# Optimization experiments

Hardware: AMD Instinct MI355X
Metric: run time of the kernel (lower is better)

## Reference

```python
import jax, jax.numpy as jnp
import numpy as np

V, D, H, L, T_BLOCK = 32000, 1024, 16, 4, 1024
HD = D // H
FF = 4 * D
EPS = 1e-5


def layer_norm(x, w, b):
    mu = jnp.mean(x, axis=-1, keepdims=True)
    var = jnp.mean(jnp.square(x - mu), axis=-1, keepdims=True)
    return (x - mu) * jax.lax.rsqrt(var + EPS) * w + b


def setup_inputs() -> dict:
    key = jax.random.key(0)
    ks = iter(jax.random.split(key, 32))
    s = 0.02
    inp = {
        "idx": jax.random.randint(next(ks), (4, 1024), 0, V, dtype=jnp.int32),
        "tok_emb": jax.random.normal(next(ks), (V, D), jnp.float32) * s,
        "pos_emb": jax.random.normal(next(ks), (T_BLOCK, D), jnp.float32) * s,
        "ln1_w": jnp.ones((L, D), jnp.float32),
        "ln1_b": jnp.zeros((L, D), jnp.float32),
        "wq": jax.random.normal(next(ks), (L, D, D), jnp.float32) * s,
        "wk": jax.random.normal(next(ks), (L, D, D), jnp.float32) * s,
        "wv": jax.random.normal(next(ks), (L, D, D), jnp.float32) * s,
        "wproj": jax.random.normal(next(ks), (L, D, D), jnp.float32) * s,
        "bproj": jnp.zeros((L, D), jnp.float32),
        "ln2_w": jnp.ones((L, D), jnp.float32),
        "ln2_b": jnp.zeros((L, D), jnp.float32),
        "w1": jax.random.normal(next(ks), (L, D, FF), jnp.float32) * s,
        "b1": jnp.zeros((L, FF), jnp.float32),
        "w2": jax.random.normal(next(ks), (L, FF, D), jnp.float32) * s,
        "b2": jnp.zeros((L, D), jnp.float32),
        "lnf_w": jnp.ones((D,), jnp.float32),
        "lnf_b": jnp.zeros((D,), jnp.float32),
        "wout": jax.random.normal(next(ks), (D, V), jnp.float32) * s,
        "bout": jnp.zeros((V,), jnp.float32),
    }
    return inp


def reference(idx, tok_emb, pos_emb, ln1_w, ln1_b, wq, wk, wv, wproj, bproj,
              ln2_w, ln2_b, w1, b1, w2, b2, lnf_w, lnf_b, wout, bout):
    B, T = idx.shape
    x = tok_emb[idx] + pos_emb[:T]  # (B,T,D)
    causal = jnp.tril(jnp.ones((T, T), bool))
    scale = 1.0 / jnp.sqrt(jnp.asarray(HD, x.dtype))
    for l in range(L):
        h = layer_norm(x, ln1_w[l], ln1_b[l])
        q = (h @ wq[l]).reshape(B, T, H, HD)
        k = (h @ wk[l]).reshape(B, T, H, HD)
        v = (h @ wv[l]).reshape(B, T, H, HD)
        scores = jnp.einsum('bqhd,bkhd->bhqk', q, k) * scale
        scores = jnp.where(causal, scores, -jnp.inf)
        weights = jax.nn.softmax(scores, axis=-1)
        attn = jnp.einsum('bhqk,bkhd->bqhd', weights, v).reshape(B, T, D)
        x = x + attn @ wproj[l] + bproj[l]
        h2 = layer_norm(x, ln2_w[l], ln2_b[l])
        x = x + jax.nn.relu(h2 @ w1[l] + b1[l]) @ w2[l] + b2[l]
    x = layer_norm(x, lnf_w, lnf_b)
    logits = x @ wout + bout  # (B,T,V)
    return logits
```

## Files before the change

### kernel.cpp

```cpp
#include <hip/hip_runtime.h>
#include <hip/hip_bf16.h>

#define V_  32000
#define D_  1024
#define H_  16
#define L_  4
#define T_  1024
#define B_  4
#define HD_ 64
#define FF_ 4096
#define M_  4096
#define QP_ 3072

typedef unsigned short u16;
typedef float  f32x4   __attribute__((ext_vector_type(4)));
typedef float  f32x16  __attribute__((ext_vector_type(16)));
typedef __bf16 bf16x8  __attribute__((ext_vector_type(8)));
typedef u16    us8     __attribute__((ext_vector_type(8)));

typedef __attribute__((address_space(1))) void gvoid;
typedef __attribute__((address_space(3))) void lvoid;

__device__ __forceinline__ void glds16(const void* g, void* l) {
  __builtin_amdgcn_global_load_lds((gvoid*)g, (lvoid*)l, 16, 0, 0);
}
__device__ __forceinline__ u16 f2bf(float f) {
  __hip_bfloat16 h = __float2bfloat16(f);
  return reinterpret_cast<u16&>(h);
}

__global__ __launch_bounds__(256) void embed_kernel(
    const int* __restrict__ idx, const float* __restrict__ tok,
    const float* __restrict__ pos, float* __restrict__ x)
{
  int bt = blockIdx.x;
  int t  = bt & (T_ - 1);
  int id = idx[bt];
  float4 a = ((const float4*)(tok + (size_t)id * D_))[threadIdx.x];
  float4 p = ((const float4*)(pos + (size_t)t  * D_))[threadIdx.x];
  a.x += p.x; a.y += p.y; a.z += p.z; a.w += p.w;
  ((float4*)(x + (size_t)bt * D_))[threadIdx.x] = a;
}

__global__ __launch_bounds__(256) void ln_kernel(
    const float* __restrict__ x, const float* __restrict__ w,
    const float* __restrict__ b, u16* __restrict__ out)
{
  int row = blockIdx.x;
  float4 v = ((const float4*)(x + (size_t)row * D_))[threadIdx.x];
  float s  = v.x + v.y + v.z + v.w;
  float s2 = v.x * v.x + v.y * v.y + v.z * v.z + v.w * v.w;
#pragma unroll
  for (int m = 1; m < 64; m <<= 1) { s += __shfl_xor(s, m); s2 += __shfl_xor(s2, m); }
  __shared__ float ssum[4], ssum2[4];
  int wv = threadIdx.x >> 6;
  if ((threadIdx.x & 63) == 0) { ssum[wv] = s; ssum2[wv] = s2; }
  __syncthreads();
  s  = ssum[0]  + ssum[1]  + ssum[2]  + ssum[3];
  s2 = ssum2[0] + ssum2[1] + ssum2[2] + ssum2[3];
  float mu  = s * (1.f / D_);
  float var = s2 * (1.f / D_) - mu * mu;
  float rs  = rsqrtf(var + 1e-5f);
  float4 wv4 = ((const float4*)w)[threadIdx.x];
  float4 bv4 = ((const float4*)b)[threadIdx.x];
  u16* o = out + (size_t)row * D_ + threadIdx.x * 4;
  o[0] = f2bf((v.x - mu) * rs * wv4.x + bv4.x);
  o[1] = f2bf((v.y - mu) * rs * wv4.y + bv4.y);
  o[2] = f2bf((v.z - mu) * rs * wv4.z + bv4.z);
  o[3] = f2bf((v.w - mu) * rs * wv4.w + bv4.w);
}

__global__ __launch_bounds__(256) void transpose_convert(
    const float* __restrict__ in, u16* __restrict__ out, int R, int C,
    size_t inStride, size_t outStride)
{
  __shared__ float tile[32][33];
  in  += (size_t)blockIdx.z * inStride;
  out += (size_t)blockIdx.z * outStride;
  int c  = blockIdx.x * 32 + threadIdx.x;
  int r0 = blockIdx.y * 32;
#pragma unroll
  for (int j = 0; j < 4; j++)
    tile[threadIdx.y + 8 * j][threadIdx.x] =
        in[(size_t)(r0 + threadIdx.y + 8 * j) * C + c];
  __syncthreads();
  int rr = r0 + threadIdx.x;
  int cb = blockIdx.x * 32;
#pragma unroll
  for (int j = 0; j < 4; j++)
    out[(size_t)(cb + threadIdx.y + 8 * j) * R + rr] =
        f2bf(tile[threadIdx.x][threadIdx.y + 8 * j]);
}

__global__ __launch_bounds__(256) void vtrans_kernel(
    const u16* __restrict__ qkv, u16* __restrict__ vtb)
{
  __shared__ u16 tile[64][72];
  int tt = blockIdx.x, bh = blockIdx.y;
  int b = bh >> 4, h = bh & 15;
  const u16* src = qkv + ((size_t)(b * T_ + tt * 64)) * QP_ + 2 * D_ + h * HD_;
#pragma unroll
  for (int it = 0; it < 2; it++) {
    int u = it * 256 + threadIdx.x;
    int r = u >> 3, c = (u & 7) << 3;
    *(us8*)&tile[r][c] = *(const us8*)&src[(size_t)r * QP_ + c];
  }
  __syncthreads();
#pragma unroll
  for (int it = 0; it < 2; it++) {
    int u = it * 256 + threadIdx.x;
    int d = u >> 3, t8 = (u & 7) << 3;
    us8 v;
#pragma unroll
    for (int j = 0; j < 8; j++) v[j] = tile[t8 + j][d];
    *(us8*)&vtb[((size_t)bh * HD_ + d) * T_ + tt * 64 + t8] = v;
  }
}

template<int EPI>
__global__ __launch_bounds__(256) void gemm_bt(
    const u16* __restrict__ A, const u16* __restrict__ Bt,
    const float* __restrict__ bias, const float* __restrict__ resid,
    void* __restrict__ Cout, int M, int N, int K)
{
  __shared__ u16 As[128 * 32];
  __shared__ u16 Bs[128 * 32];
  const int tid = threadIdx.x;
  const int m0 = blockIdx.x * 128;
  const int n0 = blockIdx.y * 128;
  const int w = tid >> 6, lane = tid & 63, lg = lane >> 4, lr = lane & 15;
  const int wr = w >> 1, wc = w & 1;
  f32x4 acc[4][4] = {};
  const int srow = tid >> 2;
  const int scol = (tid & 3) << 3;
  const u16* ap = A  + (size_t)(m0 + srow) * K + scol;
  const u16* bp = Bt + (size_t)(n0 + srow) * K + scol;
  u16* alds  = &As[tid * 8];
  u16* alds2 = &As[2048 + tid * 8];
  u16* blds  = &Bs[tid * 8];
  u16* blds2 = &Bs[2048 + tid * 8];
  for (int k0 = 0; k0 < K; k0 += 32) {
    __syncthreads();
    glds16(ap + k0,                  alds);
    glds16(ap + (size_t)64 * K + k0, alds2);
    glds16(bp + k0,                  blds);
    glds16(bp + (size_t)64 * K + k0, blds2);
    __syncthreads();
    bf16x8 af[4], bfr[4];
#pragma unroll
    for (int i = 0; i < 4; i++)
      af[i] = *(const bf16x8*)&As[(wr * 64 + i * 16 + lr) * 32 + lg * 8];
#pragma unroll
    for (int j = 0; j < 4; j++)
      bfr[j] = *(const bf16x8*)&Bs[(wc * 64 + j * 16 + lr) * 32 + lg * 8];
#pragma unroll
    for (int i = 0; i < 4; i++)
#pragma unroll
      for (int j = 0; j < 4; j++)
        acc[i][j] = __builtin_amdgcn_mfma_f32_16x16x32_bf16(af[i], bfr[j], acc[i][j], 0, 0, 0);
  }
#pragma unroll
  for (int i = 0; i < 4; i++) {
#pragma unroll
    for (int j = 0; j < 4; j++) {
      int col = n0 + wc * 64 + j * 16 + lr;
      float bv = bias ? bias[col] : 0.f;
#pragma unroll
      for (int r = 0; r < 4; r++) {
        int row = m0 + wr * 64 + i * 16 + lg * 4 + r;
        float val = acc[i][j][r] + bv;
        size_t o = (size_t)row * N + col;
        if (EPI == 0)      ((u16*)Cout)[o]   = f2bf(val);
        else if (EPI == 1) ((u16*)Cout)[o]   = f2bf(val > 0.f ? val : 0.f);
        else if (EPI == 2) ((float*)Cout)[o] = resid[o] + val;
        else               ((float*)Cout)[o] = val;
      }
    }
  }
}

#define BAR() __builtin_amdgcn_s_barrier()
#define VMC(n) asm volatile("s_waitcnt vmcnt(" #n ")" ::: "memory")
#define LGKMC(n) do { asm volatile("s_waitcnt lgkmcnt(" #n ")" ::: "memory"); \
                      __builtin_amdgcn_sched_barrier(0); } while (0)

#define CLUSTER(AF, BV, MS) do { \
  __builtin_amdgcn_s_setprio(1); \
  _Pragma("unroll") for (int mq_ = 0; mq_ < 2; ++mq_) \
  _Pragma("unroll") for (int nq_ = 0; nq_ < 2; ++nq_) \
  _Pragma("unroll") for (int kq_ = 0; kq_ < 2; ++kq_) \
    acc[(MS)+mq_][nq_] = __builtin_amdgcn_mfma_f32_32x32x16_bf16( \
        AF[mq_][kq_], BV[nq_][kq_], acc[(MS)+mq_][nq_], 0, 0, 0); \
  __builtin_amdgcn_s_setprio(0); \
} while (0)

template<int EPI>
__global__ __launch_bounds__(512, 2) void gemm256(
    const u16* __restrict__ A, const u16* __restrict__ Bt,
    const float* __restrict__ bias, void* __restrict__ Cout, int N, int K)
{
  extern __shared__ char smem[];
  const int tid = threadIdx.x;
  const int nwg = gridDim.x;
  const int orig = blockIdx.x;
  const int qq = nwg >> 3, rr = nwg & 7, xcd = orig & 7, lid = orig >> 3;
  const int swz = (xcd < rr ? xcd * (qq + 1) : rr * (qq + 1) + (xcd - rr) * qq) + lid;
  const int m0 = (swz & 15) << 8;
  const int n0 = (swz >> 4) << 8;
  const int NT = K >> 6;

  const int wid = tid >> 6, lane = tid & 63;
  const int wr = wid >> 2, wc = wid & 3;
  const int l31 = lane & 31, lh = lane >> 5;
  const int gsw = (lane & 7) ^ ((lane >> 3) & 3);
  const int srow = tid >> 3, sslot = tid & 7;
  const int sg = (srow & 7) ^ ((srow >> 3) & 3);
  const int scol = ((sslot ^ sg) << 3);
  const u16* Ag = A  + (size_t)(m0 + srow) * K + scol;
  const u16* Bg = Bt + (size_t)(n0 + srow) * K + scol;
  char* ldst = smem + tid * 16;

  auto stA = [&](int bb, int kt, int h) {
    const u16* g = Ag + (size_t)(h << 7) * K + (kt << 6);
    char* l = ldst + bb * 65536 + h * 16384;
    glds16(g, l);
    glds16(g + ((size_t)K << 6), l + 8192);
  };
  auto stB = [&](int bb, int kt, int h) {
    const u16* g = Bg + (size_t)(h << 7) * K + (kt << 6);
    char* l = ldst + bb * 65536 + 32768 + h * 16384;
    glds16(g, l);
    glds16(g + ((size_t)K << 6), l + 8192);
  };
  auto ldA = [&](int bb, int mf, int ks) {
    return *(const bf16x8*)(smem + bb * 65536 +
        ((wr * 128 + mf * 32 + l31) << 7) + (((ks * 2 + lh) ^ gsw) << 4));
  };
  auto ldB = [&](int bb, int nf, int ks) {
    return *(const bf16x8*)(smem + bb * 65536 + 32768 +
        ((wc * 64 + nf * 32 + l31) << 7) + (((ks * 2 + lh) ^ gsw) << 4));
  };

  f32x16 acc[4][2] = {};
  bf16x8 afA[2][2], afB[2][2], bfvA[2][2], bfvB[2][2];

  stA(0, 0, 0); stA(0, 0, 1); stB(0, 0, 0); stB(0, 0, 1);
  VMC(0); BAR();

  for (int t = 0; t < NT; ++t) {
    const int bb = t & 1;
    if (t + 1 < NT) {
      stA(bb ^ 1, t + 1, 0); stA(bb ^ 1, t + 1, 1);
      stB(bb ^ 1, t + 1, 0); stB(bb ^ 1, t + 1, 1);
    }
#pragma unroll
    for (int i = 0; i < 2; i++) {
      afA[i][0]  = ldA(bb, i, 0);     afA[i][1]  = ldA(bb, i, 1);
      bfvA[i][0] = ldB(bb, i, 0);     bfvA[i][1] = ldB(bb, i, 1);
    }
#pragma unroll
    for (int i = 0; i < 2; i++) { afB[i][0] = ldA(bb, 2 + i, 0); afB[i][1] = ldA(bb, 2 + i, 1); }
    LGKMC(4);
    CLUSTER(afA, bfvA, 0);
#pragma unroll
    for (int i = 0; i < 2; i++) { bfvB[i][0] = ldB(bb, i, 2); bfvB[i][1] = ldB(bb, i, 3); }
#pragma unroll
    for (int i = 0; i < 2; i++) { afA[i][0] = ldA(bb, i, 2); afA[i][1] = ldA(bb, i, 3); }
    LGKMC(8);
    CLUSTER(afB, bfvA, 2);
#pragma unroll
    for (int i = 0; i < 2; i++) { afB[i][0] = ldA(bb, 2 + i, 2); afB[i][1] = ldA(bb, 2 + i, 3); }
    LGKMC(4);
    CLUSTER(afA, bfvB, 0);
    LGKMC(0);
    CLUSTER(afB, bfvB, 2);
    VMC(0); BAR();
  }

#pragma unroll
  for (int nf = 0; nf < 2; ++nf) {
    const int col = n0 + wc * 64 + nf * 32 + l31;
    const float bv = bias ? bias[col] : 0.f;
#pragma unroll
    for (int mf = 0; mf < 4; ++mf) {
#pragma unroll
      for (int v = 0; v < 16; ++v) {
        const int row = m0 + wr * 128 + mf * 32 + (v & 3) + 8 * (v >> 2) + 4 * lh;
        float val = acc[mf][nf][v] + bv;
        size_t o = (size_t)row * N + col;
        if (EPI == 0)      ((u16*)Cout)[o]   = f2bf(val);
        else if (EPI == 1) ((u16*)Cout)[o]   = f2bf(val > 0.f ? val : 0.f);
        else               ((float*)Cout)[o] = val;
      }
    }
  }
}

__global__ __launch_bounds__(512) void attn_kernel(
    const u16* __restrict__ qkv, const u16* __restrict__ vtb,
    u16* __restrict__ o)
{
  __shared__ u16 Ks[2][64][64];
  __shared__ u16 Vs[2][64][64];
  __shared__ u16 Ps[8][16][72];
  const int qt = blockIdx.x;
  const int bh = blockIdx.y;
  const int b = bh >> 4, h = bh & 15;
  const int tid = threadIdx.x;
  const int w = tid >> 6, lane = tid & 63, lg = lane >> 4, lr = lane & 15;
  const int q0 = qt * 128;
  const size_t qbase = ((size_t)b * T_) * QP_ + h * HD_;
  const size_t obase = ((size_t)b * T_) * D_ + h * HD_;
  const u16* qb = qkv + qbase;
  const u16* kb = qkv + qbase + D_;
  const u16* vtbh = vtb + (size_t)bh * HD_ * T_;
  bf16x8 qf[2];
  const int qrow = q0 + w * 16 + lr;
#pragma unroll
  for (int ks = 0; ks < 2; ks++)
    qf[ks] = *(const bf16x8*)&qb[(size_t)qrow * QP_ + ks * 32 + lg * 8];
  f32x4 oacc[4] = {};
  float mrun[4] = {-1e30f, -1e30f, -1e30f, -1e30f};
  float lrun[4] = {0.f, 0.f, 0.f, 0.f};
  const int srow = tid >> 3, sslot = tid & 7;
  const int sg = (srow & 7) ^ ((srow >> 3) & 3);
  const int scol = (sslot ^ sg) << 3;
  u16* kdst = &Ks[0][0][0] + tid * 8;
  u16* vdst = &Vs[0][0][0] + tid * 8;
  auto stage = [&](int kt, int bb) {
    glds16(kb + (size_t)(kt * 64 + srow) * QP_ + scol, kdst + bb * 4096);
    glds16(vtbh + (size_t)srow * T_ + kt * 64 + scol, vdst + bb * 4096);
  };
  auto ldK = [&](int bb, int j, int ks) {
    int r = j * 16 + lr;
    int g = (r & 7) ^ ((r >> 3) & 3);
    return *(const bf16x8*)&Ks[bb][r][((ks * 4 + lg) ^ g) << 3];
  };
  auto ldV = [&](int bb, int jd, int ks) {
    int r = jd * 16 + lr;
    int g = (r & 7) ^ ((r >> 3) & 3);
    return *(const bf16x8*)&Vs[bb][r][((ks * 4 + lg) ^ g) << 3];
  };

  const int ktmax = 2 * qt + 1;
  stage(0, 0);
  VMC(0); BAR();
  for (int kt = 0; kt <= ktmax; kt++) {
    const int bb = kt & 1;
    if (kt < ktmax) stage(kt + 1, bb ^ 1);
    f32x4 s[4] = {};
#pragma unroll
    for (int ks = 0; ks < 2; ks++)
#pragma unroll
      for (int j = 0; j < 4; j++)
        s[j] = __builtin_amdgcn_mfma_f32_16x16x32_bf16(qf[ks], ldK(bb, j, ks), s[j], 0, 0, 0);
#pragma unroll
    for (int j = 0; j < 4; j++) {
      int key = kt * 64 + j * 16 + lr;
#pragma unroll
      for (int r = 0; r < 4; r++) {
        int qr = q0 + w * 16 + lg * 4 + r;
        s[j][r] = (key <= qr) ? s[j][r] * 0.125f : -1e30f;
      }
    }
    float al[4];
#pragma unroll
    for (int r = 0; r < 4; r++) {
      float t0 = fmaxf(fmaxf(s[0][r], s[1][r]), fmaxf(s[2][r], s[3][r]));
#pragma unroll
      for (int m = 1; m < 16; m <<= 1) t0 = fmaxf(t0, __shfl_xor(t0, m));
      float mnew = fmaxf(mrun[r], t0);
      al[r] = __expf(mrun[r] - mnew);
      mrun[r] = mnew;
    }
#pragma unroll
    for (int j = 0; j < 4; j++)
#pragma unroll
      for (int r = 0; r < 4; r++)
        s[j][r] = __expf(s[j][r] - mrun[r]);
#pragma unroll
    for (int r = 0; r < 4; r++) {
      float rs = s[0][r] + s[1][r] + s[2][r] + s[3][r];
#pragma unroll
      for (int m = 1; m < 16; m <<= 1) rs += __shfl_xor(rs, m);
      lrun[r] = lrun[r] * al[r] + rs;
#pragma unroll
      for (int jd = 0; jd < 4; jd++) oacc[jd][r] *= al[r];
    }
#pragma unroll
    for (int j = 0; j < 4; j++)
#pragma unroll
      for (int r = 0; r < 4; r++)
        Ps[w][lg * 4 + r][j * 16 + lr] = f2bf(s[j][r]);
    asm volatile("s_waitcnt lgkmcnt(0)" ::: "memory");
    __builtin_amdgcn_sched_barrier(0);
#pragma unroll
    for (int ks = 0; ks < 2; ks++) {
      bf16x8 pf = *(const bf16x8*)&Ps[w][lr][ks * 32 + lg * 8];
#pragma unroll
      for (int jd = 0; jd < 4; jd++)
        oacc[jd] = __builtin_amdgcn_mfma_f32_16x16x32_bf16(pf, ldV(bb, jd, ks), oacc[jd], 0, 0, 0);
    }
    VMC(0); BAR();
  }
#pragma unroll
  for (int jd = 0; jd < 4; jd++)
#pragma unroll
    for (int r = 0; r < 4; r++) {
      int row = q0 + w * 16 + lg * 4 + r;
      o[obase + (size_t)row * D_ + jd * 16 + lr] = f2bf(oacc[jd][r] / lrun[r]);
    }
}

extern "C" void kernel_launch(void* const* d_in, const int* in_sizes, int n_in,
                              void* d_out, int out_size, void* d_ws, size_t ws_size,
                              hipStream_t stream)
{
  const int*   idx   = (const int*)  d_in[0];
  const float* tok   = (const float*)d_in[1];
  const float* pos   = (const float*)d_in[2];
  const float* ln1w  = (const float*)d_in[3];
  const float* ln1b  = (const float*)d_in[4];
  const float* wq    = (const float*)d_in[5];
  const float* wk    = (const float*)d_in[6];
  const float* wvw   = (const float*)d_in[7];
  const float* wproj = (const float*)d_in[8];
  const float* bproj = (const float*)d_in[9];
  const float* ln2w  = (const float*)d_in[10];
  const float* ln2b  = (const float*)d_in[11];
  const float* w1    = (const float*)d_in[12];
  const float* b1    = (const float*)d_in[13];
  const float* w2    = (const float*)d_in[14];
  const float* b2    = (const float*)d_in[15];
  const float* lnfw  = (const float*)d_in[16];
  const float* lnfb  = (const float*)d_in[17];
  const float* wout  = (const float*)d_in[18];
  const float* bout  = (const float*)d_in[19];

  hipFuncSetAttribute(reinterpret_cast<const void*>(&gemm256<0>),
                      hipFuncAttributeMaxDynamicSharedMemorySize, 131072);
  hipFuncSetAttribute(reinterpret_cast<const void*>(&gemm256<1>),
                      hipFuncAttributeMaxDynamicSharedMemorySize, 131072);
  hipFuncSetAttribute(reinterpret_cast<const void*>(&gemm256<3>),
                      hipFuncAttributeMaxDynamicSharedMemorySize, 131072);

  char* ws = (char*)d_ws;
  size_t off = 0;
  auto alloc = [&](size_t bytes) {
    void* p = ws + off;
    off += (bytes + 255) & ~(size_t)255;
    return p;
  };
  u16* wqkvT  = (u16*)alloc((size_t)L_ * 3 * D_ * D_ * 2);
  u16* wprojT = (u16*)alloc((size_t)L_ * D_ * D_ * 2);
  u16* w1T    = (u16*)alloc((size_t)L_ * D_ * FF_ * 2);
  u16* w2T    = (u16*)alloc((size_t)L_ * D_ * FF_ * 2);
  u16* woutT  = (u16*)alloc((size_t)D_ * V_ * 2);
  float* x    = (float*)alloc((size_t)M_ * D_ * 4);
  u16* hbuf   = (u16*)alloc((size_t)M_ * D_ * 2);
  u16* qkvbuf = (u16*)alloc((size_t)M_ * QP_ * 2);
  u16* vtb    = (u16*)alloc((size_t)B_ * H_ * HD_ * T_ * 2);
  u16* abuf   = (u16*)alloc((size_t)M_ * D_ * 2);
  u16* f1buf  = (u16*)alloc((size_t)M_ * FF_ * 2);

  dim3 tb(32, 8);
  const size_t DD = (size_t)D_ * D_, DF = (size_t)D_ * FF_;
  transpose_convert<<<dim3(D_ / 32, D_ / 32, L_), tb, 0, stream>>>(wq,    wqkvT,          D_,  D_, DD, 3 * DD);
  transpose_convert<<<dim3(D_ / 32, D_ / 32, L_), tb, 0, stream>>>(wk,    wqkvT + DD,     D_,  D_, DD, 3 * DD);
  transpose_convert<<<dim3(D_ / 32, D_ / 32, L_), tb, 0, stream>>>(wvw,   wqkvT + 2 * DD, D_,  D_, DD, 3 * DD);
  transpose_convert<<<dim3(D_ / 32, D_ / 32, L_), tb, 0, stream>>>(wproj, wprojT,         D_,  D_, DD, DD);
  transpose_convert<<<dim3(FF_ / 32, D_ / 32, L_), tb, 0, stream>>>(w1,   w1T,            D_,  FF_, DF, DF);
  transpose_convert<<<dim3(D_ / 32, FF_ / 32, L_), tb, 0, stream>>>(w2,   w2T,            FF_, D_, DF, DF);
  transpose_convert<<<dim3(V_ / 32, D_ / 32, 1),  tb, 0, stream>>>(wout,  woutT,          D_,  V_, 0, 0);

  embed_kernel<<<M_, 256, 0, stream>>>(idx, tok, pos, x);

  dim3 gD(M_ / 128, D_ / 128);
  for (int l = 0; l < L_; l++) {
    size_t wo = (size_t)l * DD;
    size_t fo = (size_t)l * DF;
    ln_kernel<<<M_, 256, 0, stream>>>(x, ln1w + l * D_, ln1b + l * D_, hbuf);
    gemm256<0><<<dim3(16 * (QP_ / 256)), 512, 131072, stream>>>(
        hbuf, wqkvT + (size_t)l * 3 * DD, nullptr, qkvbuf, QP_, D_);
    vtrans_kernel<<<dim3(T_ / 64, B_ * H_), 256, 0, stream>>>(qkvbuf, vtb);
    attn_kernel<<<dim3(T_ / 128, B_ * H_), 512, 0, stream>>>(qkvbuf, vtb, abuf);
    gemm_bt<2><<<gD, 256, 0, stream>>>(abuf, wprojT + wo, bproj + l * D_, x, x, M_, D_, D_);
    ln_kernel<<<M_, 256, 0, stream>>>(x, ln2w + l * D_, ln2b + l * D_, hbuf);
    gemm256<1><<<dim3(16 * (FF_ / 256)), 512, 131072, stream>>>(
        hbuf, w1T + fo, b1 + l * FF_, f1buf, FF_, D_);
    gemm_bt<2><<<gD, 256, 0, stream>>>(f1buf, w2T + fo, b2 + l * D_, x, x, M_, D_, FF_);
  }
  ln_kernel<<<M_, 256, 0, stream>>>(x, lnfw, lnfb, hbuf);
  gemm256<3><<<dim3(16 * (V_ / 256)), 512, 131072, stream>>>(
      hbuf, woutT, bout, d_out, V_, D_);
}
```

Measured before the change: 1.634 ms.

## Load GEMM A operand directly from global into registers, stage only B in LDS

The 256x256 GEMM kernel stops staging the A tile through shared memory. Each wave now loads its A fragments straight from global memory into registers, prefetching the next K-step between MFMA phases, while only B is double-buffered in LDS. This halves LDS footprint (64KB instead of 128KB) and LDS read traffic. It also switches from 32x32x16 to 16x16x32 MFMA and makes the tile order row-major over N. In exchange, A reads become uncoalesced per-lane global loads that are duplicated across the four waves sharing a row block, and register pressure grows with 32 f32x4 accumulators plus A and B fragments.

```diff
diff --git a/kernel.cpp b/kernel.cpp
--- a/kernel.cpp
+++ b/kernel.cpp
@@ -28,6 +28,11 @@
   __hip_bfloat16 h = __float2bfloat16(f);
   return reinterpret_cast<u16&>(h);
 }
+
+#define BAR() __builtin_amdgcn_s_barrier()
+#define VMC(n) asm volatile("s_waitcnt vmcnt(" #n ")" ::: "memory")
+#define LGKMC(n) do { asm volatile("s_waitcnt lgkmcnt(" #n ")" ::: "memory"); \
+                      __builtin_amdgcn_sched_barrier(0); } while (0)
 
 __global__ __launch_bounds__(256) void embed_kernel(
     const int* __restrict__ idx, const float* __restrict__ tok,
@@ -179,23 +184,8 @@
   }
 }
 
-#define BAR() __builtin_amdgcn_s_barrier()
-#define VMC(n) asm volatile("s_waitcnt vmcnt(" #n ")" ::: "memory")
-#define LGKMC(n) do { asm volatile("s_waitcnt lgkmcnt(" #n ")" ::: "memory"); \
-                      __builtin_amdgcn_sched_barrier(0); } while (0)
-
-#define CLUSTER(AF, BV, MS) do { \
-  __builtin_amdgcn_s_setprio(1); \
-  _Pragma("unroll") for (int mq_ = 0; mq_ < 2; ++mq_) \
-  _Pragma("unroll") for (int nq_ = 0; nq_ < 2; ++nq_) \
-  _Pragma("unroll") for (int kq_ = 0; kq_ < 2; ++kq_) \
-    acc[(MS)+mq_][nq_] = __builtin_amdgcn_mfma_f32_32x32x16_bf16( \
-        AF[mq_][kq_], BV[nq_][kq_], acc[(MS)+mq_][nq_], 0, 0, 0); \
-  __builtin_amdgcn_s_setprio(0); \
-} while (0)
-
 template<int EPI>
-__global__ __launch_bounds__(512, 2) void gemm256(
+__global__ __launch_bounds__(512, 2) void gemm256g(
     const u16* __restrict__ A, const u16* __restrict__ Bt,
     const float* __restrict__ bias, void* __restrict__ Cout, int N, int K)
 {
@@ -205,88 +195,104 @@
   const int orig = blockIdx.x;
   const int qq = nwg >> 3, rr = nwg & 7, xcd = orig & 7, lid = orig >> 3;
   const int swz = (xcd < rr ? xcd * (qq + 1) : rr * (qq + 1) + (xcd - rr) * qq) + lid;
-  const int m0 = (swz & 15) << 8;
-  const int n0 = (swz >> 4) << 8;
+  const unsigned ntiles = (unsigned)N >> 8;
+  const int m0 = (int)((unsigned)swz / ntiles) << 8;
+  const int n0 = (int)((unsigned)swz % ntiles) << 8;
   const int NT = K >> 6;
 
   const int wid = tid >> 6, lane = tid & 63;
   const int wr = wid >> 2, wc = wid & 3;
-  const int l31 = lane & 31, lh = lane >> 5;
-  const int gsw = (lane & 7) ^ ((lane >> 3) & 3);
+  const int l15 = lane & 15, lq = lane >> 4;
+
+  const u16* Arow = A + (size_t)(m0 + wr * 128 + l15) * K + lq * 8;
+
   const int srow = tid >> 3, sslot = tid & 7;
   const int sg = (srow & 7) ^ ((srow >> 3) & 3);
   const int scol = ((sslot ^ sg) << 3);
-  const u16* Ag = A  + (size_t)(m0 + srow) * K + scol;
   const u16* Bg = Bt + (size_t)(n0 + srow) * K + scol;
   char* ldst = smem + tid * 16;
-
-  auto stA = [&](int bb, int kt, int h) {
-    const u16* g = Ag + (size_t)(h << 7) * K + (kt << 6);
-    char* l = ldst + bb * 65536 + h * 16384;
-    glds16(g, l);
-    glds16(g + ((size_t)K << 6), l + 8192);
+  auto stB = [&](int bb, int kt) {
+#pragma unroll
+    for (int j = 0; j < 4; j++)
+      glds16(Bg + (size_t)(j * 64) * K + (kt << 6), ldst + bb * 32768 + j * 8192);
   };
-  auto stB = [&](int bb, int kt, int h) {
-    const u16* g = Bg + (size_t)(h << 7) * K + (kt << 6);
-    char* l = ldst + bb * 65536 + 32768 + h * 16384;
-    glds16(g, l);
-    glds16(g + ((size_t)K << 6), l + 8192);
+  const int brow = wc * 64 + l15;
+  auto ldB = [&](int bb, int nf, int ks) {
+    int r = brow + nf * 16;
+    int g = (r & 7) ^ ((r >> 3) & 3);
+    return *(const bf16x8*)(smem + bb * 32768 + (r << 7) + ((((ks << 2) + lq) ^ g) << 4));
   };
-  auto ldA = [&](int bb, int mf, int ks) {
-    return *(const bf16x8*)(smem + bb * 65536 +
-        ((wr * 128 + mf * 32 + l31) << 7) + (((ks * 2 + lh) ^ gsw) << 4));
-  };
-  auto ldB = [&](int bb, int nf, int ks) {
-    return *(const bf16x8*)(smem + bb * 65536 + 32768 +
-        ((wc * 64 + nf * 32 + l31) << 7) + (((ks * 2 + lh) ^ gsw) << 4));
-  };
-
-  f32x16 acc[4][2] = {};
-  bf16x8 afA[2][2], afB[2][2], bfvA[2][2], bfvB[2][2];
-
-  stA(0, 0, 0); stA(0, 0, 1); stB(0, 0, 0); stB(0, 0, 1);
-  VMC(0); BAR();
+
+  f32x4 acc[8][4] = {};
+  bf16x8 a0[4][2], a1[4][2], bf[4][2];
+
+  stB(0, 0);
+#pragma unroll
+  for (int mf = 0; mf < 4; mf++)
+#pragma unroll
+    for (int ks = 0; ks < 2; ks++) {
+      a0[mf][ks] = *(const bf16x8*)(Arow + (size_t)(mf * 16) * K + ks * 32);
+      a1[mf][ks] = *(const bf16x8*)(Arow + (size_t)((mf + 4) * 16) * K + ks * 32);
+    }
+  VMC(16); BAR();
 
   for (int t = 0; t < NT; ++t) {
     const int bb = t & 1;
-    if (t + 1 < NT) {
-      stA(bb ^ 1, t + 1, 0); stA(bb ^ 1, t + 1, 1);
-      stB(bb ^ 1, t + 1, 0); stB(bb ^ 1, t + 1, 1);
-    }
-#pragma unroll
-    for (int i = 0; i < 2; i++) {
-      afA[i][0]  = ldA(bb, i, 0);     afA[i][1]  = ldA(bb, i, 1);
-      bfvA[i][0] = ldB(bb, i, 0);     bfvA[i][1] = ldB(bb, i, 1);
-    }
-#pragma unroll
-    for (int i = 0; i < 2; i++) { afB[i][0] = ldA(bb, 2 + i, 0); afB[i][1] = ldA(bb, 2 + i, 1); }
-    LGKMC(4);
-    CLUSTER(afA, bfvA, 0);
-#pragma unroll
-    for (int i = 0; i < 2; i++) { bfvB[i][0] = ldB(bb, i, 2); bfvB[i][1] = ldB(bb, i, 3); }
-#pragma unroll
-    for (int i = 0; i < 2; i++) { afA[i][0] = ldA(bb, i, 2); afA[i][1] = ldA(bb, i, 3); }
-    LGKMC(8);
-    CLUSTER(afB, bfvA, 2);
-#pragma unroll
-    for (int i = 0; i < 2; i++) { afB[i][0] = ldA(bb, 2 + i, 2); afB[i][1] = ldA(bb, 2 + i, 3); }
-    LGKMC(4);
-    CLUSTER(afA, bfvB, 0);
+    const bool sn = (t + 1 < NT);
+    if (sn) stB(bb ^ 1, t + 1);
+#pragma unroll
+    for (int nf = 0; nf < 4; nf++)
+#pragma unroll
+      for (int ks = 0; ks < 2; ks++)
+        bf[nf][ks] = ldB(bb, nf, ks);
     LGKMC(0);
-    CLUSTER(afB, bfvB, 2);
-    VMC(0); BAR();
-  }
-
-#pragma unroll
-  for (int nf = 0; nf < 2; ++nf) {
-    const int col = n0 + wc * 64 + nf * 32 + l31;
+    __builtin_amdgcn_s_setprio(1);
+#pragma unroll
+    for (int mf = 0; mf < 4; mf++)
+#pragma unroll
+      for (int nf = 0; nf < 4; nf++)
+#pragma unroll
+        for (int ks = 0; ks < 2; ks++)
+          acc[mf][nf] = __builtin_amdgcn_mfma_f32_16x16x32_bf16(
+              a0[mf][ks], bf[nf][ks], acc[mf][nf], 0, 0, 0);
+    __builtin_amdgcn_s_setprio(0);
+    if (sn) {
+#pragma unroll
+      for (int mf = 0; mf < 4; mf++)
+#pragma unroll
+        for (int ks = 0; ks < 2; ks++)
+          a0[mf][ks] = *(const bf16x8*)(Arow + (size_t)(mf * 16) * K + ((t + 1) << 6) + ks * 32);
+    }
+    __builtin_amdgcn_s_setprio(1);
+#pragma unroll
+    for (int mf = 0; mf < 4; mf++)
+#pragma unroll
+      for (int nf = 0; nf < 4; nf++)
+#pragma unroll
+        for (int ks = 0; ks < 2; ks++)
+          acc[4 + mf][nf] = __builtin_amdgcn_mfma_f32_16x16x32_bf16(
+              a1[mf][ks], bf[nf][ks], acc[4 + mf][nf], 0, 0, 0);
+    __builtin_amdgcn_s_setprio(0);
+    if (sn) {
+#pragma unroll
+      for (int mf = 0; mf < 4; mf++)
+#pragma unroll
+        for (int ks = 0; ks < 2; ks++)
+          a1[mf][ks] = *(const bf16x8*)(Arow + (size_t)((mf + 4) * 16) * K + ((t + 1) << 6) + ks * 32);
+      VMC(16); BAR();
+    }
+  }
+
+#pragma unroll
+  for (int j = 0; j < 4; j++) {
+    const int col = n0 + wc * 64 + j * 16 + l15;
     const float bv = bias ? bias[col] : 0.f;
 #pragma unroll
-    for (int mf = 0; mf < 4; ++mf) {
-#pragma unroll
-      for (int v = 0; v < 16; ++v) {
-        const int row = m0 + wr * 128 + mf * 32 + (v & 3) + 8 * (v >> 2) + 4 * lh;
-        float val = acc[mf][nf][v] + bv;
+    for (int i = 0; i < 8; i++) {
+#pragma unroll
+      for (int r = 0; r < 4; r++) {
+        const int row = m0 + wr * 128 + i * 16 + lq * 4 + r;
+        float val = acc[i][j][r] + bv;
         size_t o = (size_t)row * N + col;
         if (EPI == 0)      ((u16*)Cout)[o]   = f2bf(val);
         else if (EPI == 1) ((u16*)Cout)[o]   = f2bf(val > 0.f ? val : 0.f);
@@ -437,12 +443,12 @@
   const float* wout  = (const float*)d_in[18];
   const float* bout  = (const float*)d_in[19];
 
-  hipFuncSetAttribute(reinterpret_cast<const void*>(&gemm256<0>),
-                      hipFuncAttributeMaxDynamicSharedMemorySize, 131072);
-  hipFuncSetAttribute(reinterpret_cast<const void*>(&gemm256<1>),
-                      hipFuncAttributeMaxDynamicSharedMemorySize, 131072);
-  hipFuncSetAttribute(reinterpret_cast<const void*>(&gemm256<3>),
-                      hipFuncAttributeMaxDynamicSharedMemorySize, 131072);
+  hipFuncSetAttribute(reinterpret_cast<const void*>(&gemm256g<0>),
+                      hipFuncAttributeMaxDynamicSharedMemorySize, 65536);
+  hipFuncSetAttribute(reinterpret_cast<const void*>(&gemm256g<1>),
+                      hipFuncAttributeMaxDynamicSharedMemorySize, 65536);
+  hipFuncSetAttribute(reinterpret_cast<const void*>(&gemm256g<3>),
+                      hipFuncAttributeMaxDynamicSharedMemorySize, 65536);
 
   char* ws = (char*)d_ws;
   size_t off = 0;
@@ -480,17 +486,17 @@
     size_t wo = (size_t)l * DD;
     size_t fo = (size_t)l * DF;
     ln_kernel<<<M_, 256, 0, stream>>>(x, ln1w + l * D_, ln1b + l * D_, hbuf);
-    gemm256<0><<<dim3(16 * (QP_ / 256)), 512, 131072, stream>>>(
+    gemm256g<0><<<dim3(16 * (QP_ / 256)), 512, 65536, stream>>>(
         hbuf, wqkvT + (size_t)l * 3 * DD, nullptr, qkvbuf, QP_, D_);
     vtrans_kernel<<<dim3(T_ / 64, B_ * H_), 256, 0, stream>>>(qkvbuf, vtb);
     attn_kernel<<<dim3(T_ / 128, B_ * H_), 512, 0, stream>>>(qkvbuf, vtb, abuf);
     gemm_bt<2><<<gD, 256, 0, stream>>>(abuf, wprojT + wo, bproj + l * D_, x, x, M_, D_, D_);
     ln_kernel<<<M_, 256, 0, stream>>>(x, ln2w + l * D_, ln2b + l * D_, hbuf);
-    gemm256<1><<<dim3(16 * (FF_ / 256)), 512, 131072, stream>>>(
+    gemm256g<1><<<dim3(16 * (FF_ / 256)), 512, 65536, stream>>>(
         hbuf, w1T + fo, b1 + l * FF_, f1buf, FF_, D_);
     gemm_bt<2><<<gD, 256, 0, stream>>>(f1buf, w2T + fo, b2 + l * D_, x, x, M_, D_, FF_);
   }
   ln_kernel<<<M_, 256, 0, stream>>>(x, lnfw, lnfb, hbuf);
-  gemm256<3><<<dim3(16 * (V_ / 256)), 512, 131072, stream>>>(
+  gemm256g<3><<<dim3(16 * (V_ / 256)), 512, 65536, stream>>>(
       hbuf, woutT, bout, d_out, V_, D_);
 }
```

Result: slower. 2.343 ms (+43.4%).

## Use 4-stage K=32 LDS pipeline in gemm256 instead of double-buffered K=64

Applied to the files above, without the earlier changes.

Rewrites the main GEMM's K loop to use BK=32 tiles with four LDS buffers of 32KB each, prefetching three tiles ahead via global_load_lds and waiting with graded vmcnt. Previously, double buffering with BK=64 waited for the next tile every iteration. The aim is to hide global memory latency better. In exchange there are twice as many barriers per K step, and the interleaved LDS-read/MFMA clusters are replaced by a single load-then-compute phase, which may expose LDS latency.

```diff
diff --git a/kernel.cpp b/kernel.cpp
--- a/kernel.cpp
+++ b/kernel.cpp
@@ -28,6 +28,11 @@
   __hip_bfloat16 h = __float2bfloat16(f);
   return reinterpret_cast<u16&>(h);
 }
+
+#define BAR() __builtin_amdgcn_s_barrier()
+#define VMC(n) asm volatile("s_waitcnt vmcnt(" #n ")" ::: "memory")
+#define LGKMC(n) do { asm volatile("s_waitcnt lgkmcnt(" #n ")" ::: "memory"); \
+                      __builtin_amdgcn_sched_barrier(0); } while (0)
 
 __global__ __launch_bounds__(256) void embed_kernel(
     const int* __restrict__ idx, const float* __restrict__ tok,
@@ -179,21 +184,6 @@
   }
 }
 
-#define BAR() __builtin_amdgcn_s_barrier()
-#define VMC(n) asm volatile("s_waitcnt vmcnt(" #n ")" ::: "memory")
-#define LGKMC(n) do { asm volatile("s_waitcnt lgkmcnt(" #n ")" ::: "memory"); \
-                      __builtin_amdgcn_sched_barrier(0); } while (0)
-
-#define CLUSTER(AF, BV, MS) do { \
-  __builtin_amdgcn_s_setprio(1); \
-  _Pragma("unroll") for (int mq_ = 0; mq_ < 2; ++mq_) \
-  _Pragma("unroll") for (int nq_ = 0; nq_ < 2; ++nq_) \
-  _Pragma("unroll") for (int kq_ = 0; kq_ < 2; ++kq_) \
-    acc[(MS)+mq_][nq_] = __builtin_amdgcn_mfma_f32_32x32x16_bf16( \
-        AF[mq_][kq_], BV[nq_][kq_], acc[(MS)+mq_][nq_], 0, 0, 0); \
-  __builtin_amdgcn_s_setprio(0); \
-} while (0)
-
 template<int EPI>
 __global__ __launch_bounds__(512, 2) void gemm256(
     const u16* __restrict__ A, const u16* __restrict__ Bt,
@@ -207,74 +197,73 @@
   const int swz = (xcd < rr ? xcd * (qq + 1) : rr * (qq + 1) + (xcd - rr) * qq) + lid;
   const int m0 = (swz & 15) << 8;
   const int n0 = (swz >> 4) << 8;
-  const int NT = K >> 6;
+  const int NT = K >> 5;
 
   const int wid = tid >> 6, lane = tid & 63;
   const int wr = wid >> 2, wc = wid & 3;
   const int l31 = lane & 31, lh = lane >> 5;
-  const int gsw = (lane & 7) ^ ((lane >> 3) & 3);
-  const int srow = tid >> 3, sslot = tid & 7;
-  const int sg = (srow & 7) ^ ((srow >> 3) & 3);
-  const int scol = ((sslot ^ sg) << 3);
-  const u16* Ag = A  + (size_t)(m0 + srow) * K + scol;
-  const u16* Bg = Bt + (size_t)(n0 + srow) * K + scol;
-  char* ldst = smem + tid * 16;
-
-  auto stA = [&](int bb, int kt, int h) {
-    const u16* g = Ag + (size_t)(h << 7) * K + (kt << 6);
-    char* l = ldst + bb * 65536 + h * 16384;
-    glds16(g, l);
-    glds16(g + ((size_t)K << 6), l + 8192);
-  };
-  auto stB = [&](int bb, int kt, int h) {
-    const u16* g = Bg + (size_t)(h << 7) * K + (kt << 6);
-    char* l = ldst + bb * 65536 + 32768 + h * 16384;
-    glds16(g, l);
-    glds16(g + ((size_t)K << 6), l + 8192);
+
+  const int r0s = tid >> 3, r1s = r0s + 64, ss = tid & 7;
+  const int g0 = (r0s & 7) ^ ((r0s >> 3) & 3);
+  const int g1 = (r1s & 7) ^ ((r1s >> 3) & 3);
+  const int s0 = ss ^ g0, s1 = ss ^ g1;
+  const u16* aS0 = A  + (size_t)(m0 + r0s + ((s0 >> 2) << 7)) * K + (s0 & 3) * 8;
+  const u16* aS1 = A  + (size_t)(m0 + r1s + ((s1 >> 2) << 7)) * K + (s1 & 3) * 8;
+  const u16* bS0 = Bt + (size_t)(n0 + r0s + ((s0 >> 2) << 7)) * K + (s0 & 3) * 8;
+  const u16* bS1 = Bt + (size_t)(n0 + r1s + ((s1 >> 2) << 7)) * K + (s1 & 3) * 8;
+  auto stage = [&](int bb, int kt) {
+    char* base = smem + bb * 32768 + tid * 16;
+    glds16(aS0 + (kt << 5), base);
+    glds16(aS1 + (kt << 5), base + 8192);
+    glds16(bS0 + (kt << 5), base + 16384);
+    glds16(bS1 + (kt << 5), base + 16384 + 8192);
   };
   auto ldA = [&](int bb, int mf, int ks) {
-    return *(const bf16x8*)(smem + bb * 65536 +
-        ((wr * 128 + mf * 32 + l31) << 7) + (((ks * 2 + lh) ^ gsw) << 4));
+    int pr = mf * 32 + l31;
+    int g = (pr & 7) ^ ((pr >> 3) & 3);
+    int slot = ((wr << 2) | (ks << 1) | lh) ^ g;
+    return *(const bf16x8*)(smem + bb * 32768 + (pr << 7) + (slot << 4));
   };
   auto ldB = [&](int bb, int nf, int ks) {
-    return *(const bf16x8*)(smem + bb * 65536 + 32768 +
-        ((wc * 64 + nf * 32 + l31) << 7) + (((ks * 2 + lh) ^ gsw) << 4));
+    int r = wc * 64 + nf * 32 + l31;
+    int pr = r & 127, hf = r >> 7;
+    int g = (pr & 7) ^ ((pr >> 3) & 3);
+    int slot = ((hf << 2) | (ks << 1) | lh) ^ g;
+    return *(const bf16x8*)(smem + bb * 32768 + 16384 + (pr << 7) + (slot << 4));
   };
 
   f32x16 acc[4][2] = {};
-  bf16x8 afA[2][2], afB[2][2], bfvA[2][2], bfvB[2][2];
-
-  stA(0, 0, 0); stA(0, 0, 1); stB(0, 0, 0); stB(0, 0, 1);
-  VMC(0); BAR();
+  bf16x8 af[4][2], bf[2][2];
+
+  stage(0, 0); stage(1, 1); stage(2, 2);
+  VMC(8); BAR();
 
   for (int t = 0; t < NT; ++t) {
-    const int bb = t & 1;
-    if (t + 1 < NT) {
-      stA(bb ^ 1, t + 1, 0); stA(bb ^ 1, t + 1, 1);
-      stB(bb ^ 1, t + 1, 0); stB(bb ^ 1, t + 1, 1);
-    }
-#pragma unroll
-    for (int i = 0; i < 2; i++) {
-      afA[i][0]  = ldA(bb, i, 0);     afA[i][1]  = ldA(bb, i, 1);
-      bfvA[i][0] = ldB(bb, i, 0);     bfvA[i][1] = ldB(bb, i, 1);
-    }
-#pragma unroll
-    for (int i = 0; i < 2; i++) { afB[i][0] = ldA(bb, 2 + i, 0); afB[i][1] = ldA(bb, 2 + i, 1); }
-    LGKMC(4);
-    CLUSTER(afA, bfvA, 0);
-#pragma unroll
-    for (int i = 0; i < 2; i++) { bfvB[i][0] = ldB(bb, i, 2); bfvB[i][1] = ldB(bb, i, 3); }
-#pragma unroll
-    for (int i = 0; i < 2; i++) { afA[i][0] = ldA(bb, i, 2); afA[i][1] = ldA(bb, i, 3); }
-    LGKMC(8);
-    CLUSTER(afB, bfvA, 2);
-#pragma unroll
-    for (int i = 0; i < 2; i++) { afB[i][0] = ldA(bb, 2 + i, 2); afB[i][1] = ldA(bb, 2 + i, 3); }
-    LGKMC(4);
-    CLUSTER(afA, bfvB, 0);
+    const int bb = t & 3;
+    if (t + 3 < NT) stage((t + 3) & 3, t + 3);
+#pragma unroll
+    for (int mf = 0; mf < 4; mf++)
+#pragma unroll
+      for (int ks = 0; ks < 2; ks++) af[mf][ks] = ldA(bb, mf, ks);
+#pragma unroll
+    for (int nf = 0; nf < 2; nf++)
+#pragma unroll
+      for (int ks = 0; ks < 2; ks++) bf[nf][ks] = ldB(bb, nf, ks);
     LGKMC(0);
-    CLUSTER(afB, bfvB, 2);
-    VMC(0); BAR();
+    __builtin_amdgcn_s_setprio(1);
+#pragma unroll
+    for (int mf = 0; mf < 4; mf++)
+#pragma unroll
+      for (int nf = 0; nf < 2; nf++)
+#pragma unroll
+        for (int ks = 0; ks < 2; ks++)
+          acc[mf][nf] = __builtin_amdgcn_mfma_f32_32x32x16_bf16(
+              af[mf][ks], bf[nf][ks], acc[mf][nf], 0, 0, 0);
+    __builtin_amdgcn_s_setprio(0);
+    if (t + 3 < NT)      { VMC(8); }
+    else if (t + 2 < NT) { VMC(4); }
+    else                 { VMC(0); }
+    BAR();
   }
 
 #pragma unroll
```

Result: no change. 1.658 ms (+1.5%).
